# Performance work log

Hardware: AMD Instinct MI355X
Metric: run time of the kernel (lower is better)

The kernel has to match this reference:

```python
import jax, jax.numpy as jnp
import numpy as np

RATE = 22050.0 / 256.0
_RANGES = [(0.0, 0.32537674), (0.32537674, 0.47555801), (0.47555801, 0.64588683),
           (0.64588683, 1.16883525), (1.16883525, 2.17128976), (2.17128976, np.inf)]
LO = np.array([a * RATE for a, _ in _RANGES], dtype=np.float32)
HI = np.array([b * RATE for _, b in _RANGES], dtype=np.float32)
WEIGHT = 1.0
EPS = 1e-7


def _giou1d(a0, a1, b0, b1):
    # 1D GIoU between intervals [a0,a1] (GT) and [b0,b1] (pred)
    inter = jnp.clip(jnp.minimum(a1, b1) - jnp.maximum(a0, b0), 0.0)
    union = (a1 - a0) + (b1 - b0) - inter
    enclose = jnp.maximum(a1, b1) - jnp.minimum(a0, b0)
    iou = inter / (union + EPS)
    return iou - (enclose - union) / (enclose + EPS)


def _fcos_loss(regressions, annotations, anchor_levels):
    # anchor_levels: list of 6 1D point arrays. All annotations are valid and
    # belong to class_id, so the boolean class filters are identity (jit-safe).
    def per_sample(reg, ann):
        # sort GTs by interval length ascending (as in get_fcos_positives)
        order = jnp.argsort(ann[:, 1] - ann[:, 0])
        ann = ann[order]  # [G, 3]
        losses, pos_masks = [], []
        off = 0
        for i, pts in enumerate(anchor_levels):
            n = pts.shape[0]
            reg_i = reg[off:off + n]  # [n, 2]
            off += n
            l_star = pts[None, :] - ann[:, 0:1]   # [G, n]
            r_star = ann[:, 1:2] - pts[None, :]   # [G, n]
            in_box = (l_star >= 0.0) & (r_star >= 0.0)
            m = jnp.maximum(l_star, r_star)
            mask = in_box & (m >= LO[i]) & (m < HI[i])  # [G, n]
            pos = mask.any(axis=0)                 # [n]
            arg = jnp.argmax(mask, axis=0)         # first matching GT per anchor
            norm_ann = ann[arg] / (2.0 ** i)       # [n, 3] normalized annotation
            giou = _giou1d(norm_ann[:, 0], norm_ann[:, 1], reg_i[:, 0], reg_i[:, 1])
            losses.append(1.0 - giou)
            pos_masks.append(pos)
        loss = jnp.concatenate(losses)            # [A]
        pos = jnp.concatenate(pos_masks)          # [A]
        cnt = jnp.maximum(pos.sum(), 1)
        return (loss * pos).sum() / cnt * WEIGHT  # mean over positive anchors
    return jax.vmap(per_sample)(regressions, annotations)


def setup_inputs() -> dict:
    key = jax.random.key(0)
    k0, k1, k2, k3 = jax.random.split(key, 4)
    B, G, L = 8, 256, 16384
    levels = [L >> i for i in range(6)]  # 16384..512, total 32256
    A = sum(levels)
    anchors = {f"anchors_l{i}": (jnp.arange(n, dtype=jnp.float32) * float(2 ** i))
               for i, n in enumerate(levels)}
    start = jax.random.uniform(k0, (B, G), minval=0.0, maxval=float(L) - 500.0)
    length = jax.random.uniform(k1, (B, G), minval=20.0, maxval=400.0)
    annotations = jnp.stack([start, start + length, jnp.zeros((B, G))], axis=-1)
    p0 = jax.random.uniform(k2, (B, A), minval=0.0, maxval=float(L))
    w = jax.random.uniform(k3, (B, A), minval=1.0, maxval=400.0)
    regressions = jnp.stack([p0, p0 + w], axis=-1)
    out = {"regressions": regressions, "annotations": annotations, "class_id": 0}
    out.update(anchors)
    return out


def reference(regressions, annotations, anchors_l0, anchors_l1, anchors_l2,
              anchors_l3, anchors_l4, anchors_l5, class_id):
    if class_id == -1:
        raise ValueError
    anchor_levels = [anchors_l0, anchors_l1, anchors_l2, anchors_l3, anchors_l4, anchors_l5]
    return _fcos_loss(regressions, annotations, anchor_levels)
```

## Files before the change

### kernel.cpp

```cpp
#include <hip/hip_runtime.h>
#include <math.h>

#define BATCH 8
#define G 256
#define A_TOT 32256
#define NBLK 126
#define MAGIC 0x5A17C0DE5A17C0DEull

__constant__ float c_LO[6] = {
    0.0f,
    (float)(0.32537674 * (22050.0 / 256.0)),
    (float)(0.47555801 * (22050.0 / 256.0)),
    (float)(0.64588683 * (22050.0 / 256.0)),
    (float)(1.16883525 * (22050.0 / 256.0)),
    (float)(2.17128976 * (22050.0 / 256.0)),
};
__constant__ float c_HI[6] = {
    (float)(0.32537674 * (22050.0 / 256.0)),
    (float)(0.47555801 * (22050.0 / 256.0)),
    (float)(0.64588683 * (22050.0 / 256.0)),
    (float)(1.16883525 * (22050.0 / 256.0)),
    (float)(2.17128976 * (22050.0 / 256.0)),
    INFINITY,
};

__device__ __forceinline__ void scan_pair(
    const float4 v, const int j, const float p, const float lo, const float hi,
    float& bLen, int& bIdx, float& b0, float& b1)
{
    const float la = p - v.x, ra = v.y - p;
    const float ma = fmaxf(la, ra);
    const float lenA = v.y - v.x;
    if ((fminf(la, ra) >= 0.f) & (ma >= lo) & (ma < hi) & (lenA < bLen)) {
        bLen = lenA; bIdx = j; b0 = v.x; b1 = v.y;
    }
    const float lb = p - v.z, rb = v.w - p;
    const float mb = fmaxf(lb, rb);
    const float lenB = v.w - v.z;
    if ((fminf(lb, rb) >= 0.f) & (mb >= lo) & (mb < hi) & (lenB < bLen)) {
        bLen = lenB; bIdx = j + 1; b0 = v.z; b1 = v.w;
    }
}

__global__ __launch_bounds__(256) void fcos_fused_kernel(
    const float* __restrict__ reg,
    const float* __restrict__ ann,
    float2* __restrict__ partial,
    unsigned long long* __restrict__ flag,
    float* __restrict__ out)
{
    const int bid  = blockIdx.x;
    const int b    = bid / NBLK;
    const int blk  = bid % NBLK;
    const int t    = threadIdx.x;
    const int lane = t & 63;
    const int wid  = t >> 6;

    __shared__ __align__(16) float2 s_cpair[G + 4];
    __shared__ int   s_wcnt[4];
    __shared__ float s_wl[4], s_wc[4];

    const int aidx0 = blk * 256;
    int lvl, off;
    if (aidx0 < 16384)      { lvl = 0; off = 0; }
    else if (aidx0 < 24576) { lvl = 1; off = 16384; }
    else if (aidx0 < 28672) { lvl = 2; off = 24576; }
    else if (aidx0 < 30720) { lvl = 3; off = 28672; }
    else if (aidx0 < 31744) { lvl = 4; off = 30720; }
    else                    { lvl = 5; off = 31744; }

    const float lo  = c_LO[lvl];
    const float hi  = c_HI[lvl];
    const float xlo = lo - 0.01f;
    const float xhi = 2.0f * hi + 0.01f;

    const float P0 = (float)(aidx0 - off) * (float)(1 << lvl);
    const float P1 = (float)(aidx0 - off + 255) * (float)(1 << lvl);

    const float a0in = ann[(b * G + t) * 3 + 0];
    const float a1in = ann[(b * G + t) * 3 + 1];
    const float len  = a1in - a0in;
    const bool cand  = (len >= xlo) && (len < xhi) &&
                       (a1in >= P0 - 0.01f) && (a0in <= P1 + 0.01f);

    const unsigned long long vote = __ballot(cand);
    const int lanePos = __popcll(vote & ((1ull << lane) - 1ull));
    if (lane == 0) s_wcnt[wid] = __popcll(vote);
    __syncthreads();

    int base = 0, ncand = 0;
#pragma unroll
    for (int w = 0; w < 4; ++w) {
        const int c = s_wcnt[w];
        ncand += c;
        if (w < wid) base += c;
    }
    if (cand) s_cpair[base + lanePos] = make_float2(a0in, a1in);
    if (t < 4) s_cpair[ncand + t] = make_float2(3.0e30f, -3.0e30f);
    __syncthreads();

    const int   aidx = aidx0 + t;
    const float p    = (float)(aidx - off) * (float)(1 << lvl);
    const float2 rv  = reinterpret_cast<const float2*>(reg)[b * A_TOT + aidx];

    float lenA = 1.0e30f, lenB = 1.0e30f;
    int   idxA = 0x7FFFFFFF, idxB = 0x7FFFFFFF;
    float a0A = 0.f, a1A = 0.f, a0B = 0.f, a1B = 0.f;
    const int n4 = (ncand + 3) >> 2;
    const float4* pr4 = reinterpret_cast<const float4*>(s_cpair);
    for (int g = 0; g < n4; ++g) {
        const float4 va = pr4[2 * g + 0];
        const float4 vb = pr4[2 * g + 1];
        scan_pair(va, 4 * g + 0, p, lo, hi, lenA, idxA, a0A, a1A);
        scan_pair(vb, 4 * g + 2, p, lo, hi, lenB, idxB, a0B, a1B);
    }
    const bool pickB = (lenB < lenA) || ((lenB == lenA) && (idxB < idxA));
    const float bLen = pickB ? lenB : lenA;
    const float bA0  = pickB ? a0B  : a0A;
    const float bA1  = pickB ? a1B  : a1A;

    float loss = 0.f, cnt = 0.f;
    if (bLen < 1.0e30f) {
        const float scale = 1.0f / (float)(1 << lvl);
        const float a0 = bA0 * scale;
        const float a1 = bA1 * scale;
        const float inter = fmaxf(fminf(a1, rv.y) - fmaxf(a0, rv.x), 0.f);
        const float uni   = (a1 - a0) + (rv.y - rv.x) - inter;
        const float enc   = fmaxf(a1, rv.y) - fminf(a0, rv.x);
        const float iou   = inter / (uni + 1e-7f);
        const float giou  = iou - (enc - uni) / (enc + 1e-7f);
        loss = 1.0f - giou;
        cnt  = 1.0f;
    }

#pragma unroll
    for (int m = 32; m; m >>= 1) { loss += __shfl_xor(loss, m); cnt += __shfl_xor(cnt, m); }
    if (lane == 0) { s_wl[wid] = loss; s_wc[wid] = cnt; }
    __syncthreads();
    if (t == 0) {
        const float L = s_wl[0] + s_wl[1] + s_wl[2] + s_wl[3];
        const float C = s_wc[0] + s_wc[1] + s_wc[2] + s_wc[3];
        partial[bid] = make_float2(L, C);
        __hip_atomic_store(&flag[bid], MAGIC, __ATOMIC_RELEASE, __HIP_MEMORY_SCOPE_AGENT);
    }

    if (blk == 0 && wid == 0) {
        for (int i = lane; i < NBLK; i += 64) {
            while (__hip_atomic_load(&flag[b * NBLK + i], __ATOMIC_ACQUIRE,
                                     __HIP_MEMORY_SCOPE_AGENT) != MAGIC) { }
        }
        float L = 0.f, C = 0.f;
        for (int i = lane; i < NBLK; i += 64) {
            const float2 v = partial[b * NBLK + i];
            L += v.x; C += v.y;
        }
#pragma unroll
        for (int m = 32; m; m >>= 1) { L += __shfl_xor(L, m); C += __shfl_xor(C, m); }
        if (lane == 0) out[b] = L / fmaxf(C, 1.0f);
    }
}

extern "C" void kernel_launch(void* const* d_in, const int* in_sizes, int n_in,
                              void* d_out, int out_size, void* d_ws, size_t ws_size,
                              hipStream_t stream) {
    const float* reg = (const float*)d_in[0];
    const float* ann = (const float*)d_in[1];
    float* out = (float*)d_out;

    float2* partial = (float2*)d_ws;
    unsigned long long* flag =
        (unsigned long long*)((char*)d_ws + BATCH * NBLK * sizeof(float2));

    fcos_fused_kernel<<<BATCH * NBLK, 256, 0, stream>>>(reg, ann, partial, flag, out);
}
```

Measured before the change: 16.95 us.

## Use one persistent block per CU per sample, looping over anchor chunks

Shrinks the grid from 126 blocks per sample to 32 persistent blocks per sample. Each block walks a strided set of 256-anchor chunks, rebuilding the shared candidate list for each chunk and accumulating loss and count in registers. This cuts launch and block-scheduling overhead and makes the final spin-wait reduction smaller, since it now waits on 32 flags instead of 126. In exchange there are fewer concurrent waves to hide latency, work is serialized within each block with two barriers per chunk, and chunks from different pyramid levels are spread unevenly across blocks.

```diff
diff --git a/kernel.cpp b/kernel.cpp
--- a/kernel.cpp
+++ b/kernel.cpp
@@ -4,7 +4,9 @@
 #define BATCH 8
 #define G 256
 #define A_TOT 32256
-#define NBLK 126
+#define NCHUNK 126
+#define BLKS_PER_S 32
+#define GRID_BLKS (BATCH * BLKS_PER_S)
 #define MAGIC 0x5A17C0DE5A17C0DEull
 
 __constant__ float c_LO[6] = {
@@ -42,7 +44,7 @@
     }
 }
 
-__global__ __launch_bounds__(256) void fcos_fused_kernel(
+__global__ __launch_bounds__(256) void fcos_persist_kernel(
     const float* __restrict__ reg,
     const float* __restrict__ ann,
     float2* __restrict__ partial,
@@ -50,8 +52,8 @@
     float* __restrict__ out)
 {
     const int bid  = blockIdx.x;
-    const int b    = bid / NBLK;
-    const int blk  = bid % NBLK;
+    const int b    = bid >> 5;
+    const int c    = bid & 31;
     const int t    = threadIdx.x;
     const int lane = t & 63;
     const int wid  = t >> 6;
@@ -60,82 +62,89 @@
     __shared__ int   s_wcnt[4];
     __shared__ float s_wl[4], s_wc[4];
 
-    const int aidx0 = blk * 256;
-    int lvl, off;
-    if (aidx0 < 16384)      { lvl = 0; off = 0; }
-    else if (aidx0 < 24576) { lvl = 1; off = 16384; }
-    else if (aidx0 < 28672) { lvl = 2; off = 24576; }
-    else if (aidx0 < 30720) { lvl = 3; off = 28672; }
-    else if (aidx0 < 31744) { lvl = 4; off = 30720; }
-    else                    { lvl = 5; off = 31744; }
-
-    const float lo  = c_LO[lvl];
-    const float hi  = c_HI[lvl];
-    const float xlo = lo - 0.01f;
-    const float xhi = 2.0f * hi + 0.01f;
-
-    const float P0 = (float)(aidx0 - off) * (float)(1 << lvl);
-    const float P1 = (float)(aidx0 - off + 255) * (float)(1 << lvl);
-
     const float a0in = ann[(b * G + t) * 3 + 0];
     const float a1in = ann[(b * G + t) * 3 + 1];
     const float len  = a1in - a0in;
-    const bool cand  = (len >= xlo) && (len < xhi) &&
-                       (a1in >= P0 - 0.01f) && (a0in <= P1 + 0.01f);
 
-    const unsigned long long vote = __ballot(cand);
-    const int lanePos = __popcll(vote & ((1ull << lane) - 1ull));
-    if (lane == 0) s_wcnt[wid] = __popcll(vote);
-    __syncthreads();
+    float lossAcc = 0.f, cntAcc = 0.f;
 
-    int base = 0, ncand = 0;
+    for (int cc = c; cc < NCHUNK; cc += BLKS_PER_S) {
+        const int aidx0 = cc * 256;
+        int lvl, off;
+        if (aidx0 < 16384)      { lvl = 0; off = 0; }
+        else if (aidx0 < 24576) { lvl = 1; off = 16384; }
+        else if (aidx0 < 28672) { lvl = 2; off = 24576; }
+        else if (aidx0 < 30720) { lvl = 3; off = 28672; }
+        else if (aidx0 < 31744) { lvl = 4; off = 30720; }
+        else                    { lvl = 5; off = 31744; }
+
+        const float lo  = c_LO[lvl];
+        const float hi  = c_HI[lvl];
+        const float xlo = lo - 0.01f;
+        const float xhi = 2.0f * hi + 0.01f;
+        const float sc  = (float)(1 << lvl);
+
+        const float P0 = (float)(aidx0 - off) * sc;
+        const float P1 = (float)(aidx0 - off + 255) * sc;
+
+        const int   aidx = aidx0 + t;
+        const float p    = (float)(aidx - off) * sc;
+        const float2 rv  = reinterpret_cast<const float2*>(reg)[b * A_TOT + aidx];
+
+        const bool cand = (len >= xlo) && (len < xhi) &&
+                          (a1in >= P0 - 0.01f) && (a0in <= P1 + 0.01f);
+        const unsigned long long vote = __ballot(cand);
+        const int lanePos = __popcll(vote & ((1ull << lane) - 1ull));
+        if (lane == 0) s_wcnt[wid] = __popcll(vote);
+        __syncthreads();
+
+        int base = 0, ncand = 0;
 #pragma unroll
-    for (int w = 0; w < 4; ++w) {
-        const int c = s_wcnt[w];
-        ncand += c;
-        if (w < wid) base += c;
-    }
-    if (cand) s_cpair[base + lanePos] = make_float2(a0in, a1in);
-    if (t < 4) s_cpair[ncand + t] = make_float2(3.0e30f, -3.0e30f);
-    __syncthreads();
+        for (int w = 0; w < 4; ++w) {
+            const int n = s_wcnt[w];
+            ncand += n;
+            if (w < wid) base += n;
+        }
+        if (cand) s_cpair[base + lanePos] = make_float2(a0in, a1in);
+        if (t < 4) s_cpair[ncand + t] = make_float2(3.0e30f, -3.0e30f);
+        __syncthreads();
 
-    const int   aidx = aidx0 + t;
-    const float p    = (float)(aidx - off) * (float)(1 << lvl);
-    const float2 rv  = reinterpret_cast<const float2*>(reg)[b * A_TOT + aidx];
+        float lenA = 1.0e30f, lenB = 1.0e30f;
+        int   idxA = 0x7FFFFFFF, idxB = 0x7FFFFFFF;
+        float a0A = 0.f, a1A = 0.f, a0B = 0.f, a1B = 0.f;
+        const int n4 = (ncand + 3) >> 2;
+        const float4* pr4 = reinterpret_cast<const float4*>(s_cpair);
+        for (int g = 0; g < n4; ++g) {
+            const float4 va = pr4[2 * g + 0];
+            const float4 vb = pr4[2 * g + 1];
+            scan_pair(va, 4 * g + 0, p, lo, hi, lenA, idxA, a0A, a1A);
+            scan_pair(vb, 4 * g + 2, p, lo, hi, lenB, idxB, a0B, a1B);
+        }
+        const bool pickB = (lenB < lenA) || ((lenB == lenA) && (idxB < idxA));
+        const float bLen = pickB ? lenB : lenA;
+        const float bA0  = pickB ? a0B  : a0A;
+        const float bA1  = pickB ? a1B  : a1A;
 
-    float lenA = 1.0e30f, lenB = 1.0e30f;
-    int   idxA = 0x7FFFFFFF, idxB = 0x7FFFFFFF;
-    float a0A = 0.f, a1A = 0.f, a0B = 0.f, a1B = 0.f;
-    const int n4 = (ncand + 3) >> 2;
-    const float4* pr4 = reinterpret_cast<const float4*>(s_cpair);
-    for (int g = 0; g < n4; ++g) {
-        const float4 va = pr4[2 * g + 0];
-        const float4 vb = pr4[2 * g + 1];
-        scan_pair(va, 4 * g + 0, p, lo, hi, lenA, idxA, a0A, a1A);
-        scan_pair(vb, 4 * g + 2, p, lo, hi, lenB, idxB, a0B, a1B);
-    }
-    const bool pickB = (lenB < lenA) || ((lenB == lenA) && (idxB < idxA));
-    const float bLen = pickB ? lenB : lenA;
-    const float bA0  = pickB ? a0B  : a0A;
-    const float bA1  = pickB ? a1B  : a1A;
-
-    float loss = 0.f, cnt = 0.f;
-    if (bLen < 1.0e30f) {
-        const float scale = 1.0f / (float)(1 << lvl);
-        const float a0 = bA0 * scale;
-        const float a1 = bA1 * scale;
-        const float inter = fmaxf(fminf(a1, rv.y) - fmaxf(a0, rv.x), 0.f);
-        const float uni   = (a1 - a0) + (rv.y - rv.x) - inter;
-        const float enc   = fmaxf(a1, rv.y) - fminf(a0, rv.x);
-        const float iou   = inter / (uni + 1e-7f);
-        const float giou  = iou - (enc - uni) / (enc + 1e-7f);
-        loss = 1.0f - giou;
-        cnt  = 1.0f;
+        if (bLen < 1.0e30f) {
+            const float scale = 1.0f / sc;
+            const float a0 = bA0 * scale;
+            const float a1 = bA1 * scale;
+            const float inter = fmaxf(fminf(a1, rv.y) - fmaxf(a0, rv.x), 0.f);
+            const float uni   = (a1 - a0) + (rv.y - rv.x) - inter;
+            const float enc   = fmaxf(a1, rv.y) - fminf(a0, rv.x);
+            const float iou   = inter / (uni + 1e-7f);
+            const float giou  = iou - (enc - uni) / (enc + 1e-7f);
+            lossAcc += 1.0f - giou;
+            cntAcc  += 1.0f;
+        }
     }
 
 #pragma unroll
-    for (int m = 32; m; m >>= 1) { loss += __shfl_xor(loss, m); cnt += __shfl_xor(cnt, m); }
-    if (lane == 0) { s_wl[wid] = loss; s_wc[wid] = cnt; }
+    for (int m = 32; m; m >>= 1) {
+        lossAcc += __shfl_xor(lossAcc, m);
+        cntAcc  += __shfl_xor(cntAcc, m);
+    }
+    if (lane == 0) { s_wl[wid] = lossAcc; s_wc[wid] = cntAcc; }
     __syncthreads();
     if (t == 0) {
         const float L = s_wl[0] + s_wl[1] + s_wl[2] + s_wl[3];
@@ -144,15 +153,15 @@
         __hip_atomic_store(&flag[bid], MAGIC, __ATOMIC_RELEASE, __HIP_MEMORY_SCOPE_AGENT);
     }
 
-    if (blk == 0 && wid == 0) {
-        for (int i = lane; i < NBLK; i += 64) {
-            while (__hip_atomic_load(&flag[b * NBLK + i], __ATOMIC_ACQUIRE,
+    if (c == 29 && wid == 0) {
+        if (lane < BLKS_PER_S) {
+            while (__hip_atomic_load(&flag[b * BLKS_PER_S + lane], __ATOMIC_ACQUIRE,
                                      __HIP_MEMORY_SCOPE_AGENT) != MAGIC) { }
         }
         float L = 0.f, C = 0.f;
-        for (int i = lane; i < NBLK; i += 64) {
-            const float2 v = partial[b * NBLK + i];
-            L += v.x; C += v.y;
+        if (lane < BLKS_PER_S) {
+            const float2 v = partial[b * BLKS_PER_S + lane];
+            L = v.x; C = v.y;
         }
 #pragma unroll
         for (int m = 32; m; m >>= 1) { L += __shfl_xor(L, m); C += __shfl_xor(C, m); }
@@ -169,7 +178,7 @@
 
     float2* partial = (float2*)d_ws;
     unsigned long long* flag =
-        (unsigned long long*)((char*)d_ws + BATCH * NBLK * sizeof(float2));
+        (unsigned long long*)((char*)d_ws + GRID_BLKS * sizeof(float2));
 
-    fcos_fused_kernel<<<BATCH * NBLK, 256, 0, stream>>>(reg, ann, partial, flag, out);
+    fcos_persist_kernel<<<GRID_BLKS, 256, 0, stream>>>(reg, ann, partial, flag, out);
 }
```

Measured after the change: 14.74 us. 13.0% less time.
